# Performance work log

Hardware: AMD Instinct MI355X
Metric: run time of the kernel (lower is better)

Reference implementation:

```python
import jax, jax.numpy as jnp
import numpy as np

HID = 128
K = 8
G = 1024        # number of graphs (jets)
N_SV = 16       # secondary vertices per graph
N_TRK = 64      # tracks per graph


def _mlp2(x, W1, b1, W2, b2):
    # Linear -> ELU -> Linear -> ReLU (the sv/trk encoders)
    h = jax.nn.elu(x @ W1 + b1)
    return jax.nn.relu(h @ W2 + b2)


def _dynamic_edge_conv(src, dst, W, b, k):
    # DynamicEdgeConv with bipartite input (x_src, x_dst):
    #   edge_index = knn(src, dst, k) per graph (Euclidean in feature space)
    #   message    = nn(cat([x_i, x_j - x_i]))  with x_i = dst(target), x_j = src(neighbor)
    #   aggr       = max over the k neighbors of each target
    # src: [G, Ns, D], dst: [G, Nq, D]
    dots = jnp.einsum('gqd,gsd->gqs', dst, src)
    d2 = (jnp.sum(dst * dst, -1)[:, :, None] - 2.0 * dots
          + jnp.sum(src * src, -1)[:, None, :])            # [G, Nq, Ns]
    _, idx = jax.lax.top_k(-d2, k)                          # k nearest sources, [G, Nq, k]
    xj = jax.vmap(lambda s, i: s[i])(src, idx)              # gather neighbors [G, Nq, k, D]
    xi = dst[:, :, None, :]                                 # [G, Nq, 1, D]
    edge_feat = jnp.concatenate([jnp.broadcast_to(xi, xj.shape), xj - xi], axis=-1)
    msg = jax.nn.elu(edge_feat @ W + b)                     # [G, Nq, k, D]
    return jnp.max(msg, axis=2)                             # max-scatter -> [G, Nq, D]


def setup_inputs() -> dict:
    key = jax.random.key(0)
    ks = jax.random.split(key, 16)
    s = 0.05
    inp = {
        'x_sv': jax.random.normal(ks[0], (G * N_SV, 2), jnp.float32),
        'x_trk': jax.random.normal(ks[1], (G * N_TRK, 8), jnp.float32),
        # sv encoder
        'W_sv1': jax.random.normal(ks[2], (2, HID), jnp.float32) * s,
        'b_sv1': jnp.zeros((HID,), jnp.float32),
        'W_sv2': jax.random.normal(ks[3], (HID, HID), jnp.float32) * s,
        'b_sv2': jnp.zeros((HID,), jnp.float32),
        # trk encoder
        'W_trk1': jax.random.normal(ks[4], (8, HID), jnp.float32) * s,
        'b_trk1': jnp.zeros((HID,), jnp.float32),
        'W_trk2': jax.random.normal(ks[5], (HID, HID), jnp.float32) * s,
        'b_trk2': jnp.zeros((HID,), jnp.float32),
        # edge-conv MLPs (Linear(2*HID, HID) + ELU)
        'W_c1': jax.random.normal(ks[6], (2 * HID, HID), jnp.float32) * s,
        'b_c1': jnp.zeros((HID,), jnp.float32),
        'W_c2': jax.random.normal(ks[7], (2 * HID, HID), jnp.float32) * s,
        'b_c2': jnp.zeros((HID,), jnp.float32),
        # output head 128->64->32->4->1
        'W_o1': jax.random.normal(ks[8], (HID, 64), jnp.float32) * s,
        'b_o1': jnp.zeros((64,), jnp.float32),
        'W_o2': jax.random.normal(ks[9], (64, 32), jnp.float32) * s,
        'b_o2': jnp.zeros((32,), jnp.float32),
        'W_o3': jax.random.normal(ks[10], (32, 4), jnp.float32) * s,
        'b_o3': jnp.zeros((4,), jnp.float32),
        'W_o4': jax.random.normal(ks[11], (4, 1), jnp.float32) * s,
        'b_o4': jnp.zeros((1,), jnp.float32),
        # block-structured batch assignment (sorted, equal-size graphs)
        'batch_sv': jnp.arange(G * N_SV, dtype=jnp.int64 if jax.config.jax_enable_x64 else jnp.int32) // N_SV,
        'batch_trk': jnp.arange(G * N_TRK, dtype=jnp.int64 if jax.config.jax_enable_x64 else jnp.int32) // N_TRK,
    }
    return inp


def reference(x_sv, x_trk, W_sv1, b_sv1, W_sv2, b_sv2, W_trk1, b_trk1, W_trk2, b_trk2,
              W_c1, b_c1, W_c2, b_c2, W_o1, b_o1, W_o2, b_o2, W_o3, b_o3, W_o4, b_o4,
              batch_sv, batch_trk):
    # Batches are equal-size contiguous blocks (see setup_inputs), so per-graph
    # knn/gather/max are expressed as batched ops over a leading G dimension.
    sv = _mlp2(x_sv, W_sv1, b_sv1, W_sv2, b_sv2).reshape(G, N_SV, HID)
    trk = _mlp2(x_trk, W_trk1, b_trk1, W_trk2, b_trk2).reshape(G, N_TRK, HID)
    # conv_1: sources = encoded SVs, targets = encoded tracks
    f1 = _dynamic_edge_conv(sv, trk, W_c1, b_c1, K)          # [G, N_TRK, HID]
    # conv_2: sources = f1 (per-track), targets = encoded tracks
    f2 = _dynamic_edge_conv(f1, trk, W_c2, b_c2, K)          # [G, N_TRK, HID]
    # avg_pool_x with cluster == batch: mean over tracks of each graph
    pooled = jnp.mean(f2, axis=1)                            # [G, HID]
    h = jax.nn.elu(pooled @ W_o1 + b_o1)
    h = jax.nn.elu(h @ W_o2 + b_o2)
    h = jax.nn.elu(h @ W_o3 + b_o3)
    out = h @ W_o4 + b_o4                                    # [G, 1]
    batch = jnp.arange(G)
    return out, batch
```

## Files before the change

### kernel.cpp

```cpp
#include <hip/hip_runtime.h>

#define G_    1024
#define TPB   512
#define INF_F 3.4e38f

typedef __attribute__((ext_vector_type(8))) short short8;
typedef __attribute__((ext_vector_type(4))) float f32x4;

__device__ __forceinline__ float elu_fast(float x) { return x > 0.f ? x : __expf(x) - 1.f; }
__device__ __forceinline__ float elu_ref(float x)  { return x > 0.f ? x : expm1f(x); }

#define RB(r, c)     ((r)*128 + (((c) + 8*(r)) & 127))
#define BSTRIDE 132

#define FMA4(acc_, sc_, wv_) do { (acc_).x = fmaf((sc_),(wv_).x,(acc_).x); \
                                  (acc_).y = fmaf((sc_),(wv_).y,(acc_).y); \
                                  (acc_).z = fmaf((sc_),(wv_).z,(acc_).z); \
                                  (acc_).w = fmaf((sc_),(wv_).w,(acc_).w); } while(0)
#define MAX4(mm_, bb_)       do { (mm_).x = fmaxf((mm_).x,(bb_).x); \
                                  (mm_).y = fmaxf((mm_).y,(bb_).y); \
                                  (mm_).z = fmaxf((mm_).z,(bb_).z); \
                                  (mm_).w = fmaxf((mm_).w,(bb_).w); } while(0)

#define MFMA1(acc_, A_, B_) \
    acc_ = __builtin_amdgcn_mfma_f32_16x16x32_bf16((A_), (B_), (acc_), 0, 0, 0)

__device__ __forceinline__ unsigned short bf16_of(float v) {
    unsigned u = __float_as_uint(v);
    u = u + 0x7FFFu + ((u >> 16) & 1u);
    return (unsigned short)(u >> 16);
}
__device__ __forceinline__ float f32_of(unsigned short h) {
    return __uint_as_float((unsigned)h << 16);
}

__global__ void prep_pack(const float* __restrict__ Wtrk2, const float* __restrict__ Wsv2,
                          const float* __restrict__ Wc1,   const float* __restrict__ Wc2,
                          unsigned short* __restrict__ wsu) {
    const int o = blockIdx.x * 256 + threadIdx.x;
    if (o >= 6 * 16384) return;
    const int m = o >> 14, pos = o & 16383;
    const int j = pos & 7, lane = (pos >> 3) & 63, tile = pos >> 9;
    const int ks = tile >> 3, ni = tile & 7;
    const int d = ks * 32 + (lane >> 4) * 8 + j;
    const int c = ni * 16 + (lane & 15);
    const int e = d * 128 + c;
    float v;
    switch (m) {
        case 0: v = Wtrk2[e]; break;
        case 1: v = Wsv2[e]; break;
        case 2: v = Wc1[16384 + e]; break;
        case 3: v = Wc1[e] - Wc1[16384 + e]; break;
        case 4: v = Wc2[e] - Wc2[16384 + e]; break;
        default: v = Wc2[16384 + e]; break;
    }
    wsu[m * 16384 + pos] = bf16_of(v);
}

#define LOADB1(B_, m_, pos_) B_ = *(const short8*)(wsu + (m_) * 16384 + (pos_))
#define LDFRAG(buf_, r_, k0_) (*(const short8*)&(buf_)[RB((r_), (k0_))])

__global__ __launch_bounds__(TPB, 6)
void fused_mfma(const float* __restrict__ x_sv,  const float* __restrict__ x_trk,
                const float* __restrict__ W_sv1, const float* __restrict__ b_sv1,
                const float* __restrict__ b_sv2,
                const float* __restrict__ W_trk1,const float* __restrict__ b_trk1,
                const float* __restrict__ b_trk2,
                const float* __restrict__ b_c1,  const float* __restrict__ b_c2,
                const float* __restrict__ W_o1,  const float* __restrict__ b_o1,
                const float* __restrict__ W_o2,  const float* __restrict__ b_o2,
                const float* __restrict__ W_o3,  const float* __restrict__ b_o3,
                const float* __restrict__ W_o4,  const float* __restrict__ b_o4,
                const unsigned short* __restrict__ wsu,
                float* __restrict__ out)
{
    __shared__ __align__(16) char sAraw[16896];
    __shared__ __align__(16) char sBraw[16384];
    __shared__ __align__(16) char sCraw[16896];
    short*    sAh = (short*)sAraw;    float* sAf = (float*)sAraw;
    short*    sBh = (short*)sBraw;    float* sBf = (float*)sBraw;
    unsigned* sBu = (unsigned*)sBraw;
    short*    sCh = (short*)sCraw;    float* sCf = (float*)sCraw;

    const int g    = blockIdx.x;
    const int tid  = threadIdx.x;
    const int c128 = tid & 127;
    const int g4   = tid >> 7;
    const int wv   = tid >> 6;
    const int lane = tid & 63;
    const int quad = lane >> 4;
    const int ln   = lane & 15;

    sCf[2048 + tid] = x_trk[(size_t)g * 512 + tid];
    if (tid < 32) sCf[2560 + tid] = x_sv[(size_t)g * 32 + tid];
    __syncthreads();

    {
        float w[8];
        #pragma unroll
        for (int k = 0; k < 8; k++) w[k] = W_trk1[k * 128 + c128];
        const float b1 = b_trk1[c128];
        #pragma unroll
        for (int i = 0; i < 16; i++) {
            const int r = g4 * 16 + i;
            float xr[8];
            *(float4*)&xr[0] = *(const float4*)&sCf[2048 + r * 8];
            *(float4*)&xr[4] = *(const float4*)&sCf[2048 + r * 8 + 4];
            float acc = b1;
            #pragma unroll
            for (int k = 0; k < 8; k++) acc = fmaf(xr[k], w[k], acc);
            sBh[RB(r, c128)] = bf16_of(elu_fast(acc));
        }
    }
    __syncthreads();

    {
        const int mi = wv >> 1, nb = (wv & 1) * 4;
        const int row = mi * 16 + ln;
        f32x4 acc[4];
        #pragma unroll
        for (int t = 0; t < 4; t++) {
            const float bz = b_trk2[(nb + t) * 16 + ln];
            acc[t] = (f32x4){bz, bz, bz, bz};
        }
        #pragma unroll 2
        for (int ks = 0; ks < 4; ks++) {
            const int k0 = ks * 32 + quad * 8;
            const short8 A = LDFRAG(sBh, row, k0);
            #pragma unroll
            for (int t = 0; t < 4; t++) {
                const int pos = ((ks * 8 + (nb + t)) * 64 + lane) * 8;
                short8 B;
                LOADB1(B, 0, pos);
                MFMA1(acc[t], A, B);
            }
        }
        #pragma unroll
        for (int t = 0; t < 4; t++)
            #pragma unroll
            for (int r = 0; r < 4; r++)
                sAh[RB(mi * 16 + quad * 4 + r, (nb + t) * 16 + ln)] =
                    bf16_of(fmaxf(acc[t][r], 0.f));
    }
    __syncthreads();

    {
        const float w0 = W_sv1[c128], w1 = W_sv1[128 + c128];
        const float b1 = b_sv1[c128];
        #pragma unroll
        for (int i = 0; i < 4; i++) {
            const int s = g4 * 4 + i;
            sBh[RB(s, c128)] = bf16_of(
                elu_fast(fmaf(sCf[2560 + s * 2 + 1], w1, fmaf(sCf[2560 + s * 2], w0, b1))));
        }
    }
    __syncthreads();

    {
        const int ni = wv;
        const float bz = b_sv2[ni * 16 + ln];
        f32x4 acc = (f32x4){bz, bz, bz, bz};
        #pragma unroll 2
        for (int ks = 0; ks < 4; ks++) {
            const int k0 = ks * 32 + quad * 8;
            const short8 A = LDFRAG(sBh, ln, k0);
            const int pos = ((ks * 8 + ni) * 64 + lane) * 8;
            short8 B;
            LOADB1(B, 1, pos);
            MFMA1(acc, A, B);
        }
        #pragma unroll
        for (int r = 0; r < 4; r++) {
            const float v = fmaxf(acc[r], 0.f);
            sCh[RB(quad * 4 + r, ni * 16 + ln)] = bf16_of(v);
            float p = v * v;
            #pragma unroll
            for (int o = 1; o <= 8; o <<= 1) p += __shfl_xor(p, o, 16);
            if (ln == 0) sBf[2048 + ni * 16 + quad * 4 + r] = p;
        }
    }
    __syncthreads();

    {
        const int ni = wv;
        const bool doP4 = (wv < 4);
        f32x4 accB = (f32x4){0.f, 0.f, 0.f, 0.f};
        f32x4 accS = (f32x4){0.f, 0.f, 0.f, 0.f};
        #pragma unroll 2
        for (int ks = 0; ks < 4; ks++) {
            const int k0 = ks * 32 + quad * 8;
            const short8 S = LDFRAG(sCh, ln, k0);
            const int pos = ((ks * 8 + ni) * 64 + lane) * 8;
            short8 B;
            LOADB1(B, 2, pos);
            MFMA1(accB, S, B);
            if (doP4) {
                const short8 T = LDFRAG(sAh, wv * 16 + ln, k0);
                MFMA1(accS, T, S);
            }
        }
        #pragma unroll
        for (int r = 0; r < 4; r++)
            sCf[1984 + (quad * 4 + r) * BSTRIDE + ni * 16 + ln] = accB[r];
        if (doP4) {
            float nsv = 0.f;
            #pragma unroll
            for (int p = 0; p < 8; p++) nsv += sBf[2048 + p * 16 + ln];
            #pragma unroll
            for (int r = 0; r < 4; r++)
                sBf[(wv * 16 + quad * 4 + r) * 17 + ln] = fmaf(-2.f, accS[r], nsv);
        }
    }
    __syncthreads();

    {
        const int q  = tid >> 3;
        const int s0 = tid & 7;
        float sc0 = sBf[q * 17 + s0];
        float sc1 = sBf[q * 17 + s0 + 8];
        unsigned pack1 = 0u;
        #pragma unroll
        for (int r = 0; r < 8; r++) {
            float bv = sc0; int bs = s0;
            if (sc1 < bv) { bv = sc1; bs = s0 + 8; }
            #pragma unroll
            for (int o = 1; o <= 4; o <<= 1) {
                const float ov = __shfl_xor(bv, o, 8);
                const int   os = __shfl_xor(bs, o, 8);
                if (ov < bv || (ov == bv && os < bs)) { bv = ov; bs = os; }
            }
            pack1 |= (unsigned)bs << (4 * r);
            if (bs == s0)     sc0 = INF_F;
            if (bs == s0 + 8) sc1 = INF_F;
        }
        if (s0 == 0) sBu[1088 + q] = pack1;
    }
    __syncthreads();

    {
        const int mi = wv >> 1, nb = (wv & 1) * 4;
        const int row = mi * 16 + ln;
        f32x4 a1acc[4];
        #pragma unroll
        for (int t = 0; t < 4; t++) {
            const float bz1 = b_c1[(nb + t) * 16 + ln];
            a1acc[t] = (f32x4){bz1, bz1, bz1, bz1};
        }
        #pragma unroll 2
        for (int ks = 0; ks < 4; ks++) {
            const int k0 = ks * 32 + quad * 8;
            const short8 A = LDFRAG(sAh, row, k0);
            #pragma unroll
            for (int t = 0; t < 4; t++) {
                const int pos = ((ks * 8 + (nb + t)) * 64 + lane) * 8;
                short8 B;
                LOADB1(B, 3, pos);
                MFMA1(a1acc[t], A, B);
            }
        }
        unsigned pk[4];
        #pragma unroll
        for (int r = 0; r < 4; r++) pk[r] = sBu[1088 + mi * 16 + quad * 4 + r];
        __syncthreads();
        float np[4] = {0.f, 0.f, 0.f, 0.f};
        const int ccb = nb * 16 + ln;
        const float* b1base = &sCf[1984 + ccb];
        #pragma unroll
        for (int r = 0; r < 4; r++) {
            float mx0 = -INF_F, mx1 = -INF_F, mx2 = -INF_F, mx3 = -INF_F;
            #pragma unroll
            for (int j = 0; j < 8; j++) {
                const int s = (int)((pk[r] >> (4 * j)) & 15u);
                const float* rp = b1base + s * BSTRIDE;
                mx0 = fmaxf(mx0, rp[0]);
                mx1 = fmaxf(mx1, rp[16]);
                mx2 = fmaxf(mx2, rp[32]);
                mx3 = fmaxf(mx3, rp[48]);
            }
            const float mxa[4] = {mx0, mx1, mx2, mx3};
            #pragma unroll
            for (int t = 0; t < 4; t++) {
                const float f = elu_fast(a1acc[t][r] + mxa[t]);
                sBh[RB(mi * 16 + quad * 4 + r, ccb + 16 * t)] = bf16_of(f);
                np[r] = fmaf(f, f, np[r]);
            }
        }
        #pragma unroll
        for (int r = 0; r < 4; r++) {
            #pragma unroll
            for (int o = 1; o <= 8; o <<= 1) np[r] += __shfl_xor(np[r], o, 16);
            if (ln == 0) sCf[(wv & 1) * 64 + mi * 16 + quad * 4 + r] = np[r];
        }
    }
    __syncthreads();

    {
        const int mi = wv >> 1, nia = (wv & 1) * 2;
        const int row = mi * 16 + ln;
        float ns[2];
        #pragma unroll
        for (int u = 0; u < 2; u++) {
            const int s = (nia + u) * 16 + ln;
            ns[u] = sCf[s] + sCf[64 + s];
        }
        __syncthreads();
        f32x4 acc[2];
        acc[0] = (f32x4){0.f, 0.f, 0.f, 0.f};
        acc[1] = (f32x4){0.f, 0.f, 0.f, 0.f};
        #pragma unroll 2
        for (int ks = 0; ks < 4; ks++) {
            const int k0 = ks * 32 + quad * 8;
            const short8 A = LDFRAG(sAh, row, k0);
            #pragma unroll
            for (int u = 0; u < 2; u++) {
                const short8 Bf = LDFRAG(sBh, (nia + u) * 16 + ln, k0);
                MFMA1(acc[u], A, Bf);
            }
        }
        #pragma unroll
        for (int u = 0; u < 2; u++) {
            const int s = (nia + u) * 16 + ln;
            #pragma unroll
            for (int r = 0; r < 4; r++)
                sCf[(mi * 16 + quad * 4 + r) * 64 + s] = fmaf(-2.f, acc[u][r], ns[u]);
        }
    }
    __syncthreads();

    unsigned lo2, hi2;
    {
        const int q = tid >> 3;
        const int j = tid & 7;
        float v[8];
        *(float4*)&v[0] = *(const float4*)&sCf[q * 64 + 8 * j];
        *(float4*)&v[4] = *(const float4*)&sCf[q * 64 + 8 * j + 4];
        lo2 = 0u; hi2 = 0u;
        #pragma unroll
        for (int r = 0; r < 8; r++) {
            float bv = v[0]; int bs = 8 * j;
            #pragma unroll
            for (int t = 1; t < 8; t++)
                if (v[t] < bv) { bv = v[t]; bs = 8 * j + t; }
            #pragma unroll
            for (int o = 1; o <= 4; o <<= 1) {
                const float ov = __shfl_xor(bv, o, 8);
                const int   os = __shfl_xor(bs, o, 8);
                if (ov < bv || (ov == bv && os < bs)) { bv = ov; bs = os; }
            }
            if (r < 4) lo2 |= (unsigned)bs << (8 * r);
            else       hi2 |= (unsigned)bs << (8 * (r - 4));
            #pragma unroll
            for (int t = 0; t < 8; t++)
                if (bs == 8 * j + t) v[t] = INF_F;
        }
    }
    __syncthreads();

    unsigned a2p[8];
    {
        const int mi = wv >> 1, nb = (wv & 1) * 4;
        const int row = mi * 16 + ln;
        f32x4 a2acc[4];
        #pragma unroll
        for (int t = 0; t < 4; t++) {
            const float bz2 = b_c2[(nb + t) * 16 + ln];
            a2acc[t] = (f32x4){bz2, bz2, bz2, bz2};
        }
        #pragma unroll 2
        for (int ks = 0; ks < 4; ks++) {
            const int k0 = ks * 32 + quad * 8;
            const short8 A = LDFRAG(sAh, row, k0);
            #pragma unroll
            for (int t = 0; t < 4; t++) {
                const int pos = ((ks * 8 + (nb + t)) * 64 + lane) * 8;
                short8 B;
                LOADB1(B, 4, pos);
                MFMA1(a2acc[t], A, B);
            }
        }
        #pragma unroll
        for (int t = 0; t < 4; t++) {
            a2p[2 * t]     = (unsigned)bf16_of(a2acc[t][0]) |
                             ((unsigned)bf16_of(a2acc[t][1]) << 16);
            a2p[2 * t + 1] = (unsigned)bf16_of(a2acc[t][2]) |
                             ((unsigned)bf16_of(a2acc[t][3]) << 16);
        }
    }
    __syncthreads();

    {
        const int mi = wv >> 1, nb = (wv & 1) * 4;
        const int row = mi * 16 + ln;
        f32x4 acc[4];
        #pragma unroll
        for (int t = 0; t < 4; t++) acc[t] = (f32x4){0.f, 0.f, 0.f, 0.f};
        #pragma unroll 2
        for (int ks = 0; ks < 4; ks++) {
            const int k0 = ks * 32 + quad * 8;
            const short8 A = LDFRAG(sBh, row, k0);
            #pragma unroll
            for (int t = 0; t < 4; t++) {
                const int pos = ((ks * 8 + (nb + t)) * 64 + lane) * 8;
                short8 B;
                LOADB1(B, 5, pos);
                MFMA1(acc[t], A, B);
            }
        }
        float* bp = (mi < 2) ? sAf : sCf;
        const int ccb = nb * 16 + ln;
        #pragma unroll
        for (int t = 0; t < 4; t++)
            #pragma unroll
            for (int r = 0; r < 4; r++) {
                const int rr = mi * 16 + quad * 4 + r;
                bp[(rr & 31) * BSTRIDE + ccb + 16 * t] = acc[t][r];
            }
    }
    __syncthreads();

    if ((tid & 7) == 0) {
        const int q = tid >> 3;
        sBu[1024 + 2 * q]     = lo2;
        sBu[1024 + 2 * q + 1] = hi2;
    }
    __syncthreads();

    {
        const int mi = wv >> 1, nb = (wv & 1) * 4;
        float ps[4] = {0.f, 0.f, 0.f, 0.f};
        const int ccb = nb * 16 + ln;
        const float* bA = &sAf[ccb];
        const float* bC = &sCf[ccb];
        #pragma unroll
        for (int r = 0; r < 4; r++) {
            const int rr = mi * 16 + quad * 4 + r;
            const unsigned plo = sBu[1024 + 2 * rr];
            const unsigned phi = sBu[1024 + 2 * rr + 1];
            float mx0 = -INF_F, mx1 = -INF_F, mx2 = -INF_F, mx3 = -INF_F;
            #pragma unroll
            for (int j = 0; j < 8; j++) {
                const int s = (int)(((j < 4) ? (plo >> (8 * j))
                                             : (phi >> (8 * (j - 4)))) & 63u);
                const float* rp = ((s < 32) ? bA : bC) + (s & 31) * BSTRIDE;
                mx0 = fmaxf(mx0, rp[0]);
                mx1 = fmaxf(mx1, rp[16]);
                mx2 = fmaxf(mx2, rp[32]);
                mx3 = fmaxf(mx3, rp[48]);
            }
            const float mxa[4] = {mx0, mx1, mx2, mx3};
            #pragma unroll
            for (int t = 0; t < 4; t++) {
                const unsigned u = a2p[2 * t + (r >> 1)];
                const float a2v = __uint_as_float((r & 1) ? (u & 0xFFFF0000u) : (u << 16));
                ps[t] += elu_fast(a2v + mxa[t]);
            }
        }
        #pragma unroll
        for (int t = 0; t < 4; t++) {
            ps[t] += __shfl_xor(ps[t], 16, 64);
            ps[t] += __shfl_xor(ps[t], 32, 64);
        }
        if (lane < 16)
            #pragma unroll
            for (int t = 0; t < 4; t++)
                sBf[mi * 128 + (nb + t) * 16 + lane] = ps[t];
    }
    __syncthreads();

    if (tid < 128) {
        const float p = (sBf[tid] + sBf[128 + tid] + sBf[256 + tid] + sBf[384 + tid]) * (1.f / 64.f);
        sBf[512 + tid] = p;
    }
    __syncthreads();
    if (tid < 64) {
        float acc = b_o1[tid];
        for (int d = 0; d < 128; d++) acc = fmaf(sBf[512 + d], W_o1[d * 64 + tid], acc);
        sBf[640 + tid] = elu_fast(acc);
    }
    __syncthreads();
    if (tid < 32) {
        float acc = b_o2[tid];
        for (int d = 0; d < 64; d++) acc = fmaf(sBf[640 + d], W_o2[d * 32 + tid], acc);
        sBf[704 + tid] = elu_fast(acc);
    }
    __syncthreads();
    if (tid < 4) {
        float acc = b_o3[tid];
        for (int d = 0; d < 32; d++) acc = fmaf(sBf[704 + d], W_o3[d * 4 + tid], acc);
        sBf[736 + tid] = elu_fast(acc);
    }
    __syncthreads();
    if (tid == 0) {
        float acc = b_o4[0];
        #pragma unroll
        for (int d = 0; d < 4; d++) acc = fmaf(sBf[736 + d], W_o4[d], acc);
        out[g] = acc;
        out[G_ + g] = (float)g;
    }
}

#define ROTV(r, d)    ((r)*128 + (((d) + 4*(r)) & 127))
#define BS1V(s, c)    (2048 + (s)*128 + (((c) + 4*(s)) & 127))
__global__ __launch_bounds__(TPB, 2)
void fused_vec(const float* __restrict__ x_sv,  const float* __restrict__ x_trk,
               const float* __restrict__ W_sv1, const float* __restrict__ b_sv1,
               const float* __restrict__ W_sv2, const float* __restrict__ b_sv2,
               const float* __restrict__ W_trk1,const float* __restrict__ b_trk1,
               const float* __restrict__ W_trk2,const float* __restrict__ b_trk2,
               const float* __restrict__ W_c1,  const float* __restrict__ b_c1,
               const float* __restrict__ W_c2,  const float* __restrict__ b_c2,
               const float* __restrict__ W_o1,  const float* __restrict__ b_o1,
               const float* __restrict__ W_o2,  const float* __restrict__ b_o2,
               const float* __restrict__ W_o3,  const float* __restrict__ b_o3,
               const float* __restrict__ W_o4,  const float* __restrict__ b_o4,
               float* __restrict__ out)
{
    __shared__ float sA[8192];
    __shared__ float sB[8192];
    __shared__ float sC[4096];
    const int g    = blockIdx.x;
    const int tid  = threadIdx.x;
    const int c128 = tid & 127;
    const int g4   = tid >> 7;
    const int cq   = tid & 31;
    const int c0   = cq * 4;
    const int rg   = tid >> 5;
    const int lane_hi = tid & 32;

    sC[2048 + tid] = x_trk[(size_t)g * 512 + tid];
    if (tid < 32) sC[2560 + tid] = x_sv[(size_t)g * 32 + tid];
    __syncthreads();
    {
        float w[8];
        #pragma unroll
        for (int k = 0; k < 8; k++) w[k] = W_trk1[k * 128 + c128];
        const float b1 = b_trk1[c128];
        #pragma unroll
        for (int i = 0; i < 16; i++) {
            const int r = g4 * 16 + i;
            float acc = b1;
            #pragma unroll
            for (int k = 0; k < 8; k++) acc = fmaf(sC[2048 + r * 8 + k], w[k], acc);
            sB[r * 128 + c128] = elu_ref(acc);
        }
    }
    __syncthreads();
    {
        const int r0 = rg * 4;
        float4 acc[4];
        const float4 bz = *(const float4*)&b_trk2[c0];
        #pragma unroll
        for (int i = 0; i < 4; i++) acc[i] = bz;
        for (int d0 = 0; d0 < 128; d0 += 4) {
            const float4 w0 = *(const float4*)&W_trk2[(d0 + 0) * 128 + c0];
            const float4 w1 = *(const float4*)&W_trk2[(d0 + 1) * 128 + c0];
            const float4 w2 = *(const float4*)&W_trk2[(d0 + 2) * 128 + c0];
            const float4 w3 = *(const float4*)&W_trk2[(d0 + 3) * 128 + c0];
            #pragma unroll
            for (int i = 0; i < 4; i++) {
                const float4 h = *(const float4*)&sB[(r0 + i) * 128 + d0];
                FMA4(acc[i], h.x, w0); FMA4(acc[i], h.y, w1);
                FMA4(acc[i], h.z, w2); FMA4(acc[i], h.w, w3);
            }
        }
        #pragma unroll
        for (int i = 0; i < 4; i++) {
            float4 r;
            r.x = fmaxf(acc[i].x, 0.f); r.y = fmaxf(acc[i].y, 0.f);
            r.z = fmaxf(acc[i].z, 0.f); r.w = fmaxf(acc[i].w, 0.f);
            *(float4*)&sA[ROTV(r0 + i, c0)] = r;
        }
    }
    __syncthreads();
    {
        const float w0 = W_sv1[c128], w1 = W_sv1[128 + c128];
        const float b1 = b_sv1[c128];
        #pragma unroll
        for (int i = 0; i < 4; i++) {
            const int s = g4 * 4 + i;
            sB[s * 128 + c128] =
                elu_ref(fmaf(sC[2560 + s * 2 + 1], w1, fmaf(sC[2560 + s * 2], w0, b1)));
        }
    }
    __syncthreads();
    {
        const int s = rg;
        float4 acc = *(const float4*)&b_sv2[c0];
        for (int d0 = 0; d0 < 128; d0 += 4) {
            const float4 w0 = *(const float4*)&W_sv2[(d0 + 0) * 128 + c0];
            const float4 w1 = *(const float4*)&W_sv2[(d0 + 1) * 128 + c0];
            const float4 w2 = *(const float4*)&W_sv2[(d0 + 2) * 128 + c0];
            const float4 w3 = *(const float4*)&W_sv2[(d0 + 3) * 128 + c0];
            const float4 h = *(const float4*)&sB[s * 128 + d0];
            FMA4(acc, h.x, w0); FMA4(acc, h.y, w1);
            FMA4(acc, h.z, w2); FMA4(acc, h.w, w3);
        }
        float4 r;
        r.x = fmaxf(acc.x, 0.f); r.y = fmaxf(acc.y, 0.f);
        r.z = fmaxf(acc.z, 0.f); r.w = fmaxf(acc.w, 0.f);
        *(float4*)&sC[ROTV(s, c0)] = r;
    }
    __syncthreads();
    unsigned pack1;
    {
        {
            const int s = rg;
            float4 acc = {0.f, 0.f, 0.f, 0.f};
            for (int d0 = 0; d0 < 128; d0 += 4) {
                const float4 e  = *(const float4*)&sC[ROTV(s, d0)];
                const float4 w0 = *(const float4*)&W_c1[(128 + d0 + 0) * 128 + c0];
                const float4 w1 = *(const float4*)&W_c1[(128 + d0 + 1) * 128 + c0];
                const float4 w2 = *(const float4*)&W_c1[(128 + d0 + 2) * 128 + c0];
                const float4 w3 = *(const float4*)&W_c1[(128 + d0 + 3) * 128 + c0];
                FMA4(acc, e.x, w0); FMA4(acc, e.y, w1);
                FMA4(acc, e.z, w2); FMA4(acc, e.w, w3);
            }
            *(float4*)&sC[BS1V(s, c0)] = acc;
        }
        const int q  = tid >> 3;
        const int s0 = tid & 7;
        float d0a = 0.f, d1a = 0.f, n0 = 0.f, n1 = 0.f;
        for (int d0 = 0; d0 < 128; d0 += 4) {
            const float4 t  = *(const float4*)&sA[ROTV(q, d0)];
            const float4 v0 = *(const float4*)&sC[ROTV(s0, d0)];
            const float4 v1 = *(const float4*)&sC[ROTV(s0 + 8, d0)];
            d0a += t.x * v0.x + t.y * v0.y + t.z * v0.z + t.w * v0.w;
            d1a += t.x * v1.x + t.y * v1.y + t.z * v1.z + t.w * v1.w;
            n0  += v0.x * v0.x + v0.y * v0.y + v0.z * v0.z + v0.w * v0.w;
            n1  += v1.x * v1.x + v1.y * v1.y + v1.z * v1.z + v1.w * v1.w;
        }
        float sc0 = fmaf(-2.f, d0a, n0);
        float sc1 = fmaf(-2.f, d1a, n1);
        pack1 = 0u;
        #pragma unroll
        for (int r = 0; r < 8; r++) {
            float bv = sc0; int bs = s0;
            if (sc1 < bv) { bv = sc1; bs = s0 + 8; }
            #pragma unroll
            for (int o = 1; o <= 4; o <<= 1) {
                const float ov = __shfl_xor(bv, o, 8);
                const int   os = __shfl_xor(bs, o, 8);
                if (ov < bv || (ov == bv && os < bs)) { bv = ov; bs = os; }
            }
            pack1 |= (unsigned)bs << (4 * r);
            if (bs == s0)     sc0 = INF_F;
            if (bs == s0 + 8) sc1 = INF_F;
        }
    }
    __syncthreads();
    float4 a2v[4];
    {
        const int q0 = rg * 4;
        float4 a1[4];
        const float4 bc1 = *(const float4*)&b_c1[c0];
        const float4 bc2 = *(const float4*)&b_c2[c0];
        #pragma unroll
        for (int i = 0; i < 4; i++) { a1[i] = bc1; a2v[i] = bc2; }
        for (int d0 = 0; d0 < 128; d0 += 4) {
            float4 t[4];
            #pragma unroll
            for (int i = 0; i < 4; i++) t[i] = *(const float4*)&sA[ROTV(q0 + i, d0)];
            #pragma unroll
            for (int dj = 0; dj < 4; dj++) {
                float4 wv;
                const float4 wa = *(const float4*)&W_c1[(d0 + dj) * 128 + c0];
                const float4 wb = *(const float4*)&W_c1[(128 + d0 + dj) * 128 + c0];
                wv.x = wa.x - wb.x; wv.y = wa.y - wb.y;
                wv.z = wa.z - wb.z; wv.w = wa.w - wb.w;
                FMA4(a1[0], ((const float*)&t[0])[dj], wv);
                FMA4(a1[1], ((const float*)&t[1])[dj], wv);
                FMA4(a1[2], ((const float*)&t[2])[dj], wv);
                FMA4(a1[3], ((const float*)&t[3])[dj], wv);
            }
            #pragma unroll
            for (int dj = 0; dj < 4; dj++) {
                float4 wv;
                const float4 wa = *(const float4*)&W_c2[(d0 + dj) * 128 + c0];
                const float4 wb = *(const float4*)&W_c2[(128 + d0 + dj) * 128 + c0];
                wv.x = wa.x - wb.x; wv.y = wa.y - wb.y;
                wv.z = wa.z - wb.z; wv.w = wa.w - wb.w;
                FMA4(a2v[0], ((const float*)&t[0])[dj], wv);
                FMA4(a2v[1], ((const float*)&t[1])[dj], wv);
                FMA4(a2v[2], ((const float*)&t[2])[dj], wv);
                FMA4(a2v[3], ((const float*)&t[3])[dj], wv);
            }
        }
        #pragma unroll
        for (int i = 0; i < 4; i++) {
            const int q = q0 + i;
            const unsigned pk = __shfl(pack1, 8 * i + lane_hi);
            float4 m = {-INF_F, -INF_F, -INF_F, -INF_F};
            #pragma unroll
            for (int j = 0; j < 8; j++) {
                const int s = (int)((pk >> (4 * j)) & 15u);
                const float4 b = *(const float4*)&sC[BS1V(s, c0)];
                MAX4(m, b);
            }
            float4 f;
            f.x = elu_ref(a1[i].x + m.x); f.y = elu_ref(a1[i].y + m.y);
            f.z = elu_ref(a1[i].z + m.z); f.w = elu_ref(a1[i].w + m.w);
            *(float4*)&sB[ROTV(q, c0)] = f;
        }
    }
    __syncthreads();
    {
        const int s  = tid & 63;
        const int q0 = (tid >> 6) * 8;
        float acc[8];
        #pragma unroll
        for (int i = 0; i < 8; i++) acc[i] = 0.f;
        float nrm = 0.f;
        for (int d0 = 0; d0 < 128; d0 += 4) {
            const float4 f = *(const float4*)&sB[ROTV(s, d0)];
            nrm = fmaf(f.x, f.x, nrm); nrm = fmaf(f.y, f.y, nrm);
            nrm = fmaf(f.z, f.z, nrm); nrm = fmaf(f.w, f.w, nrm);
            #pragma unroll
            for (int i = 0; i < 8; i++) {
                const float4 t = *(const float4*)&sA[ROTV(q0 + i, d0)];
                acc[i] = fmaf(t.x, f.x, acc[i]); acc[i] = fmaf(t.y, f.y, acc[i]);
                acc[i] = fmaf(t.z, f.z, acc[i]); acc[i] = fmaf(t.w, f.w, acc[i]);
            }
        }
        #pragma unroll
        for (int i = 0; i < 8; i++)
            sC[(q0 + i) * 64 + s] = fmaf(-2.f, acc[i], nrm);
    }
    __syncthreads();
    unsigned lo2, hi2;
    {
        const int q = tid >> 3;
        const int j = tid & 7;
        float v[8];
        *(float4*)&v[0] = *(const float4*)&sC[q * 64 + 8 * j];
        *(float4*)&v[4] = *(const float4*)&sC[q * 64 + 8 * j + 4];
        lo2 = 0u; hi2 = 0u;
        #pragma unroll
        for (int r = 0; r < 8; r++) {
            float bv = v[0]; int bs = 8 * j;
            #pragma unroll
            for (int t = 1; t < 8; t++)
                if (v[t] < bv) { bv = v[t]; bs = 8 * j + t; }
            #pragma unroll
            for (int o = 1; o <= 4; o <<= 1) {
                const float ov = __shfl_xor(bv, o, 8);
                const int   os = __shfl_xor(bs, o, 8);
                if (ov < bv || (ov == bv && os < bs)) { bv = ov; bs = os; }
            }
            if (r < 4) lo2 |= (unsigned)bs << (8 * r);
            else       hi2 |= (unsigned)bs << (8 * (r - 4));
            #pragma unroll
            for (int t = 0; t < 8; t++)
                if (bs == 8 * j + t) v[t] = INF_F;
        }
        const int r0 = rg * 4;
        float4 acc[4];
        #pragma unroll
        for (int i = 0; i < 4; i++) acc[i] = make_float4(0.f, 0.f, 0.f, 0.f);
        for (int d0 = 0; d0 < 128; d0 += 4) {
            const float4 w0 = *(const float4*)&W_c2[(128 + d0 + 0) * 128 + c0];
            const float4 w1 = *(const float4*)&W_c2[(128 + d0 + 1) * 128 + c0];
            const float4 w2 = *(const float4*)&W_c2[(128 + d0 + 2) * 128 + c0];
            const float4 w3 = *(const float4*)&W_c2[(128 + d0 + 3) * 128 + c0];
            #pragma unroll
            for (int i = 0; i < 4; i++) {
                const float4 f = *(const float4*)&sB[ROTV(r0 + i, d0)];
                FMA4(acc[i], f.x, w0); FMA4(acc[i], f.y, w1);
                FMA4(acc[i], f.z, w2); FMA4(acc[i], f.w, w3);
            }
        }
        #pragma unroll
        for (int i = 0; i < 4; i++)
            *(float4*)&sA[ROTV(r0 + i, c0)] = acc[i];
    }
    __syncthreads();
    {
        const int q0 = rg * 4;
        float4 ps = {0.f, 0.f, 0.f, 0.f};
        #pragma unroll
        for (int i = 0; i < 4; i++) {
            const unsigned plo = __shfl(lo2, 8 * i + lane_hi);
            const unsigned phi = __shfl(hi2, 8 * i + lane_hi);
            float4 m = {-INF_F, -INF_F, -INF_F, -INF_F};
            #pragma unroll
            for (int j = 0; j < 8; j++) {
                const int s = (int)(((j < 4) ? (plo >> (8 * j)) : (phi >> (8 * (j - 4)))) & 63u);
                const float4 b = *(const float4*)&sA[ROTV(s, c0)];
                MAX4(m, b);
            }
            ps.x += elu_ref(a2v[i].x + m.x); ps.y += elu_ref(a2v[i].y + m.y);
            ps.z += elu_ref(a2v[i].z + m.z); ps.w += elu_ref(a2v[i].w + m.w);
        }
        *(float4*)&sB[rg * 128 + c0] = ps;
    }
    __syncthreads();
    if (tid < 128) {
        float p = 0.f;
        #pragma unroll
        for (int t = 0; t < 16; t++) p += sB[t * 128 + tid];
        sB[2048 + tid] = p * (1.f / 64.f);
    }
    __syncthreads();
    if (tid < 64) {
        float acc = b_o1[tid];
        for (int d = 0; d < 128; d++) acc = fmaf(sB[2048 + d], W_o1[d * 64 + tid], acc);
        sB[2176 + tid] = elu_ref(acc);
    }
    __syncthreads();
    if (tid < 32) {
        float acc = b_o2[tid];
        for (int d = 0; d < 64; d++) acc = fmaf(sB[2176 + d], W_o2[d * 32 + tid], acc);
        sB[2240 + tid] = elu_ref(acc);
    }
    __syncthreads();
    if (tid < 4) {
        float acc = b_o3[tid];
        for (int d = 0; d < 32; d++) acc = fmaf(sB[2240 + d], W_o3[d * 4 + tid], acc);
        sB[2272 + tid] = elu_ref(acc);
    }
    __syncthreads();
    if (tid == 0) {
        float acc = b_o4[0];
        #pragma unroll
        for (int d = 0; d < 4; d++) acc = fmaf(sB[2272 + d], W_o4[d], acc);
        out[g] = acc;
        out[G_ + g] = (float)g;
    }
}

extern "C" void kernel_launch(void* const* d_in, const int* in_sizes, int n_in,
                              void* d_out, int out_size, void* d_ws, size_t ws_size,
                              hipStream_t stream) {
    const float* x_sv   = (const float*)d_in[0];
    const float* x_trk  = (const float*)d_in[1];
    const float* W_sv1  = (const float*)d_in[2];
    const float* b_sv1  = (const float*)d_in[3];
    const float* W_sv2  = (const float*)d_in[4];
    const float* b_sv2  = (const float*)d_in[5];
    const float* W_trk1 = (const float*)d_in[6];
    const float* b_trk1 = (const float*)d_in[7];
    const float* W_trk2 = (const float*)d_in[8];
    const float* b_trk2 = (const float*)d_in[9];
    const float* W_c1   = (const float*)d_in[10];
    const float* b_c1   = (const float*)d_in[11];
    const float* W_c2   = (const float*)d_in[12];
    const float* b_c2   = (const float*)d_in[13];
    const float* W_o1   = (const float*)d_in[14];
    const float* b_o1   = (const float*)d_in[15];
    const float* W_o2   = (const float*)d_in[16];
    const float* b_o2   = (const float*)d_in[17];
    const float* W_o3   = (const float*)d_in[18];
    const float* b_o3   = (const float*)d_in[19];
    const float* W_o4   = (const float*)d_in[20];
    const float* b_o4   = (const float*)d_in[21];
    float* out = (float*)d_out;

    const size_t WS_NEED = (size_t)6 * 16384 * sizeof(unsigned short);
    if (ws_size >= WS_NEED && d_ws != nullptr) {
        unsigned short* wsu = (unsigned short*)d_ws;
        prep_pack<<<384, 256, 0, stream>>>(W_trk2, W_sv2, W_c1, W_c2, wsu);
        fused_mfma<<<G_, TPB, 0, stream>>>(x_sv, x_trk, W_sv1, b_sv1, b_sv2,
                                           W_trk1, b_trk1, b_trk2, b_c1, b_c2,
                                           W_o1, b_o1, W_o2, b_o2, W_o3, b_o3,
                                           W_o4, b_o4, wsu, out);
    } else {
        fused_vec<<<G_, TPB, 0, stream>>>(x_sv, x_trk, W_sv1, b_sv1, W_sv2, b_sv2,
                                          W_trk1, b_trk1, W_trk2, b_trk2,
                                          W_c1, b_c1, W_c2, b_c2,
                                          W_o1, b_o1, W_o2, b_o2, W_o3, b_o3,
                                          W_o4, b_o4, out);
    }
}
```

Measured before the change: 164.6 us.

## Shrink shared memory footprint and reorder stages to raise occupancy to eight blocks

Cuts shared memory per block from about 49 KB to 40 KB by dropping the padded BSTRIDE layout, compacting buffers and reusing them differently across stages. The conv2 first-half MFMA (a2p) moves earlier and the top-k index write is merged into the selection stage. Launch bounds rise from 6 to 8 blocks per CU. Losing the row padding may add LDS bank conflicts, and the extra in-stage barriers plus tighter register limits could cause spills.

```diff
diff --git a/kernel.cpp b/kernel.cpp
--- a/kernel.cpp
+++ b/kernel.cpp
@@ -11,7 +11,6 @@
 __device__ __forceinline__ float elu_ref(float x)  { return x > 0.f ? x : expm1f(x); }
 
 #define RB(r, c)     ((r)*128 + (((c) + 8*(r)) & 127))
-#define BSTRIDE 132
 
 #define FMA4(acc_, sc_, wv_) do { (acc_).x = fmaf((sc_),(wv_).x,(acc_).x); \
                                   (acc_).y = fmaf((sc_),(wv_).y,(acc_).y); \
@@ -60,7 +59,7 @@
 #define LOADB1(B_, m_, pos_) B_ = *(const short8*)(wsu + (m_) * 16384 + (pos_))
 #define LDFRAG(buf_, r_, k0_) (*(const short8*)&(buf_)[RB((r_), (k0_))])
 
-__global__ __launch_bounds__(TPB, 6)
+__global__ __launch_bounds__(TPB, 8)
 void fused_mfma(const float* __restrict__ x_sv,  const float* __restrict__ x_trk,
                 const float* __restrict__ W_sv1, const float* __restrict__ b_sv1,
                 const float* __restrict__ b_sv2,
@@ -74,13 +73,14 @@
                 const unsigned short* __restrict__ wsu,
                 float* __restrict__ out)
 {
-    __shared__ __align__(16) char sAraw[16896];
+    __shared__ __align__(16) char sAraw[16384];
     __shared__ __align__(16) char sBraw[16384];
-    __shared__ __align__(16) char sCraw[16896];
+    __shared__ __align__(16) char sCraw[8192];
     short*    sAh = (short*)sAraw;    float* sAf = (float*)sAraw;
     short*    sBh = (short*)sBraw;    float* sBf = (float*)sBraw;
     unsigned* sBu = (unsigned*)sBraw;
     short*    sCh = (short*)sCraw;    float* sCf = (float*)sCraw;
+    unsigned* sCu = (unsigned*)sCraw;
 
     const int g    = blockIdx.x;
     const int tid  = threadIdx.x;
@@ -91,8 +91,8 @@
     const int quad = lane >> 4;
     const int ln   = lane & 15;
 
-    sCf[2048 + tid] = x_trk[(size_t)g * 512 + tid];
-    if (tid < 32) sCf[2560 + tid] = x_sv[(size_t)g * 32 + tid];
+    sCf[tid] = x_trk[(size_t)g * 512 + tid];
+    if (tid < 32) sCf[512 + tid] = x_sv[(size_t)g * 32 + tid];
     __syncthreads();
 
     {
@@ -104,8 +104,8 @@
         for (int i = 0; i < 16; i++) {
             const int r = g4 * 16 + i;
             float xr[8];
-            *(float4*)&xr[0] = *(const float4*)&sCf[2048 + r * 8];
-            *(float4*)&xr[4] = *(const float4*)&sCf[2048 + r * 8 + 4];
+            *(float4*)&xr[0] = *(const float4*)&sCf[r * 8];
+            *(float4*)&xr[4] = *(const float4*)&sCf[r * 8 + 4];
             float acc = b1;
             #pragma unroll
             for (int k = 0; k < 8; k++) acc = fmaf(xr[k], w[k], acc);
@@ -151,7 +151,7 @@
         for (int i = 0; i < 4; i++) {
             const int s = g4 * 4 + i;
             sBh[RB(s, c128)] = bf16_of(
-                elu_fast(fmaf(sCf[2560 + s * 2 + 1], w1, fmaf(sCf[2560 + s * 2], w0, b1))));
+                elu_fast(fmaf(sCf[512 + s * 2 + 1], w1, fmaf(sCf[512 + s * 2], w0, b1))));
         }
     }
     __syncthreads();
@@ -199,13 +199,16 @@
                 MFMA1(accS, T, S);
             }
         }
+        float nsv = 0.f;
+        if (doP4) {
+            #pragma unroll
+            for (int p = 0; p < 8; p++) nsv += sBf[2048 + p * 16 + ln];
+        }
+        __syncthreads();
         #pragma unroll
         for (int r = 0; r < 4; r++)
-            sCf[1984 + (quad * 4 + r) * BSTRIDE + ni * 16 + ln] = accB[r];
+            sCf[(quad * 4 + r) * 128 + ni * 16 + ln] = accB[r];
         if (doP4) {
-            float nsv = 0.f;
-            #pragma unroll
-            for (int p = 0; p < 8; p++) nsv += sBf[2048 + p * 16 + ln];
             #pragma unroll
             for (int r = 0; r < 4; r++)
                 sBf[(wv * 16 + quad * 4 + r) * 17 + ln] = fmaf(-2.f, accS[r], nsv);
@@ -264,14 +267,14 @@
         __syncthreads();
         float np[4] = {0.f, 0.f, 0.f, 0.f};
         const int ccb = nb * 16 + ln;
-        const float* b1base = &sCf[1984 + ccb];
+        const float* b1base = &sCf[ccb];
         #pragma unroll
         for (int r = 0; r < 4; r++) {
             float mx0 = -INF_F, mx1 = -INF_F, mx2 = -INF_F, mx3 = -INF_F;
             #pragma unroll
             for (int j = 0; j < 8; j++) {
                 const int s = (int)((pk[r] >> (4 * j)) & 15u);
-                const float* rp = b1base + s * BSTRIDE;
+                const float* rp = b1base + s * 128;
                 mx0 = fmaxf(mx0, rp[0]);
                 mx1 = fmaxf(mx1, rp[16]);
                 mx2 = fmaxf(mx2, rp[32]);
@@ -289,7 +292,43 @@
         for (int r = 0; r < 4; r++) {
             #pragma unroll
             for (int o = 1; o <= 8; o <<= 1) np[r] += __shfl_xor(np[r], o, 16);
-            if (ln == 0) sCf[(wv & 1) * 64 + mi * 16 + quad * 4 + r] = np[r];
+        }
+        __syncthreads();
+        if (ln == 0) {
+            #pragma unroll
+            for (int r = 0; r < 4; r++)
+                sCf[(wv & 1) * 64 + mi * 16 + quad * 4 + r] = np[r];
+        }
+    }
+
+    unsigned a2p[8];
+    {
+        const int mi = wv >> 1, nb = (wv & 1) * 4;
+        const int row = mi * 16 + ln;
+        f32x4 a2acc[4];
+        #pragma unroll
+        for (int t = 0; t < 4; t++) {
+            const float bz2 = b_c2[(nb + t) * 16 + ln];
+            a2acc[t] = (f32x4){bz2, bz2, bz2, bz2};
+        }
+        #pragma unroll 2
+        for (int ks = 0; ks < 4; ks++) {
+            const int k0 = ks * 32 + quad * 8;
+            const short8 A = LDFRAG(sAh, row, k0);
+            #pragma unroll
+            for (int t = 0; t < 4; t++) {
+                const int pos = ((ks * 8 + (nb + t)) * 64 + lane) * 8;
+                short8 B;
+                LOADB1(B, 4, pos);
+                MFMA1(a2acc[t], A, B);
+            }
+        }
+        #pragma unroll
+        for (int t = 0; t < 4; t++) {
+            a2p[2 * t]     = (unsigned)bf16_of(a2acc[t][0]) |
+                             ((unsigned)bf16_of(a2acc[t][1]) << 16);
+            a2p[2 * t + 1] = (unsigned)bf16_of(a2acc[t][2]) |
+                             ((unsigned)bf16_of(a2acc[t][3]) << 16);
         }
     }
     __syncthreads();
@@ -303,7 +342,6 @@
             const int s = (nia + u) * 16 + ln;
             ns[u] = sCf[s] + sCf[64 + s];
         }
-        __syncthreads();
         f32x4 acc[2];
         acc[0] = (f32x4){0.f, 0.f, 0.f, 0.f};
         acc[1] = (f32x4){0.f, 0.f, 0.f, 0.f};
@@ -317,24 +355,24 @@
                 MFMA1(acc[u], A, Bf);
             }
         }
+        __syncthreads();
         #pragma unroll
         for (int u = 0; u < 2; u++) {
             const int s = (nia + u) * 16 + ln;
             #pragma unroll
             for (int r = 0; r < 4; r++)
-                sCf[(mi * 16 + quad * 4 + r) * 64 + s] = fmaf(-2.f, acc[u][r], ns[u]);
-        }
-    }
-    __syncthreads();
-
-    unsigned lo2, hi2;
+                sAf[(mi * 16 + quad * 4 + r) * 64 + s] = fmaf(-2.f, acc[u][r], ns[u]);
+        }
+    }
+    __syncthreads();
+
     {
         const int q = tid >> 3;
         const int j = tid & 7;
         float v[8];
-        *(float4*)&v[0] = *(const float4*)&sCf[q * 64 + 8 * j];
-        *(float4*)&v[4] = *(const float4*)&sCf[q * 64 + 8 * j + 4];
-        lo2 = 0u; hi2 = 0u;
+        *(float4*)&v[0] = *(const float4*)&sAf[q * 64 + 8 * j];
+        *(float4*)&v[4] = *(const float4*)&sAf[q * 64 + 8 * j + 4];
+        unsigned lo2 = 0u, hi2 = 0u;
         #pragma unroll
         for (int r = 0; r < 8; r++) {
             float bv = v[0]; int bs = 8 * j;
@@ -353,37 +391,9 @@
             for (int t = 0; t < 8; t++)
                 if (bs == 8 * j + t) v[t] = INF_F;
         }
-    }
-    __syncthreads();
-
-    unsigned a2p[8];
-    {
-        const int mi = wv >> 1, nb = (wv & 1) * 4;
-        const int row = mi * 16 + ln;
-        f32x4 a2acc[4];
-        #pragma unroll
-        for (int t = 0; t < 4; t++) {
-            const float bz2 = b_c2[(nb + t) * 16 + ln];
-            a2acc[t] = (f32x4){bz2, bz2, bz2, bz2};
-        }
-        #pragma unroll 2
-        for (int ks = 0; ks < 4; ks++) {
-            const int k0 = ks * 32 + quad * 8;
-            const short8 A = LDFRAG(sAh, row, k0);
-            #pragma unroll
-            for (int t = 0; t < 4; t++) {
-                const int pos = ((ks * 8 + (nb + t)) * 64 + lane) * 8;
-                short8 B;
-                LOADB1(B, 4, pos);
-                MFMA1(a2acc[t], A, B);
-            }
-        }
-        #pragma unroll
-        for (int t = 0; t < 4; t++) {
-            a2p[2 * t]     = (unsigned)bf16_of(a2acc[t][0]) |
-                             ((unsigned)bf16_of(a2acc[t][1]) << 16);
-            a2p[2 * t + 1] = (unsigned)bf16_of(a2acc[t][2]) |
-                             ((unsigned)bf16_of(a2acc[t][3]) << 16);
+        if (j == 0) {
+            sCu[128 + 2 * q]     = lo2;
+            sCu[128 + 2 * q + 1] = hi2;
         }
     }
     __syncthreads();
@@ -406,22 +416,16 @@
                 MFMA1(acc[t], A, B);
             }
         }
-        float* bp = (mi < 2) ? sAf : sCf;
+        __syncthreads();
+        float* bp = (mi < 2) ? sAf : sBf;
         const int ccb = nb * 16 + ln;
         #pragma unroll
         for (int t = 0; t < 4; t++)
             #pragma unroll
             for (int r = 0; r < 4; r++) {
                 const int rr = mi * 16 + quad * 4 + r;
-                bp[(rr & 31) * BSTRIDE + ccb + 16 * t] = acc[t][r];
-            }
-    }
-    __syncthreads();
-
-    if ((tid & 7) == 0) {
-        const int q = tid >> 3;
-        sBu[1024 + 2 * q]     = lo2;
-        sBu[1024 + 2 * q + 1] = hi2;
+                bp[(rr & 31) * 128 + ccb + 16 * t] = acc[t][r];
+            }
     }
     __syncthreads();
 
@@ -430,18 +434,18 @@
         float ps[4] = {0.f, 0.f, 0.f, 0.f};
         const int ccb = nb * 16 + ln;
         const float* bA = &sAf[ccb];
-        const float* bC = &sCf[ccb];
+        const float* bB = &sBf[ccb];
         #pragma unroll
         for (int r = 0; r < 4; r++) {
             const int rr = mi * 16 + quad * 4 + r;
-            const unsigned plo = sBu[1024 + 2 * rr];
-            const unsigned phi = sBu[1024 + 2 * rr + 1];
+            const unsigned plo = sCu[128 + 2 * rr];
+            const unsigned phi = sCu[128 + 2 * rr + 1];
             float mx0 = -INF_F, mx1 = -INF_F, mx2 = -INF_F, mx3 = -INF_F;
             #pragma unroll
             for (int j = 0; j < 8; j++) {
                 const int s = (int)(((j < 4) ? (plo >> (8 * j))
                                              : (phi >> (8 * (j - 4)))) & 63u);
-                const float* rp = ((s < 32) ? bA : bC) + (s & 31) * BSTRIDE;
+                const float* rp = ((s < 32) ? bA : bB) + (s & 31) * 128;
                 mx0 = fmaxf(mx0, rp[0]);
                 mx1 = fmaxf(mx1, rp[16]);
                 mx2 = fmaxf(mx2, rp[32]);
@@ -460,6 +464,7 @@
             ps[t] += __shfl_xor(ps[t], 16, 64);
             ps[t] += __shfl_xor(ps[t], 32, 64);
         }
+        __syncthreads();
         if (lane < 16)
             #pragma unroll
             for (int t = 0; t < 4; t++)
```

After: 167.9 us. Within noise of the previous version (+2.0%).
